# Optimization experiments

Hardware: AMD Instinct MI355X
Metric: run time of the kernel (lower is better)

## Reference

```python
import jax, jax.numpy as jnp
import numpy as np

B, T, H = 8, 512, 1024
DC = 8            # concept_dim_total = 6 + 2
DIN = H + DC      # 1032
V, L = 8, 4       # op_vocab_size, prog_len


def setup_inputs() -> dict:
    key = jax.random.key(0)
    ks = jax.random.split(key, 20)
    s = 0.02
    inp = {
        "x": jax.random.normal(ks[0], (B, T, H), dtype=jnp.float32),
        # concept classifier heads
        "W_tt": jax.random.normal(ks[1], (6, H), dtype=jnp.float32) * s,
        "b_tt": jnp.zeros((6,), jnp.float32),
        "W_pol": jax.random.normal(ks[2], (2, H), dtype=jnp.float32) * s,
        "b_pol": jnp.zeros((2,), jnp.float32),
        # program generator
        "W_c2h": jax.random.normal(ks[3], (H, DIN), dtype=jnp.float32) * s,
        "b_c2h": jnp.zeros((H,), jnp.float32),
        "W_ih": jax.random.normal(ks[4], (3 * H, DIN), dtype=jnp.float32) * s,
        "W_hh": jax.random.normal(ks[5], (3 * H, H), dtype=jnp.float32) * s,
        "b_ih": jnp.zeros((3 * H,), jnp.float32),
        "b_hh": jnp.zeros((3 * H,), jnp.float32),
        "W_proj": jax.random.normal(ks[6], (V, H), dtype=jnp.float32) * s,
        "b_proj": jnp.zeros((V,), jnp.float32),
        # op library: num_ops stacked Linear(DIN->H)-GELU-Linear(H->H)
        "W1": jax.random.normal(ks[7], (V, H, DIN), dtype=jnp.float32) * s,
        "b1": jnp.zeros((V, H), jnp.float32),
        "W2": jax.random.normal(ks[8], (V, H, H), dtype=jnp.float32) * s,
        "b2": jnp.zeros((V, H), jnp.float32),
    }
    return inp


def _forward(x, W_tt, b_tt, W_pol, b_pol, W_c2h, b_c2h, W_ih, W_hh, b_ih, b_hh,
             W_proj, b_proj, W1, b1, W2, b2):
    # concept classifier
    tt = x @ W_tt.T + b_tt              # (B,T,6)
    pol = x @ W_pol.T + b_pol           # (B,T,2)
    concept_feats = jnp.concatenate([tt, pol], axis=-1)  # (B,T,8)
    concept_summary = jnp.concatenate([tt.mean(axis=1), pol.mean(axis=1)], axis=-1)  # (B,8)
    pooled = x.mean(axis=1)             # (B,H)
    context = jnp.concatenate([pooled, concept_summary], axis=-1)  # (B,DIN)

    # program generator: GRU with zero inputs, h0 from context (PyTorch gate eqs)
    h0 = context @ W_c2h.T + b_c2h      # (B,H)
    zero_in = jnp.zeros((context.shape[0], DIN), x.dtype)
    gi = zero_in @ W_ih.T + b_ih        # (B,3H); zero-input contribution = bias
    gi_r, gi_z, gi_n = jnp.split(gi, 3, axis=-1)

    def gru_step(h, _):
        gh = h @ W_hh.T + b_hh
        gh_r, gh_z, gh_n = jnp.split(gh, 3, axis=-1)
        r = jax.nn.sigmoid(gi_r + gh_r)
        z = jax.nn.sigmoid(gi_z + gh_z)
        n = jnp.tanh(gi_n + r * gh_n)
        h_new = (1.0 - z) * n + z * h
        return h_new, h_new

    _, hs = jax.lax.scan(gru_step, h0, None, length=L)   # (L,B,H)
    rnn_out = jnp.transpose(hs, (1, 0, 2))               # (B,L,H)
    program_logits = rnn_out @ W_proj.T + b_proj         # (B,L,V)

    # op library: outputs are identical across L, so compute each op once and
    # average the softmax weights over L (exact same math as expand+mean).
    x_aug = jnp.concatenate([x, concept_feats], axis=-1)           # (B,T,DIN)
    hmid = jax.nn.gelu(jnp.einsum('btd,vhd->btvh', x_aug, W1) + b1, approximate=False)
    op_out = jnp.einsum('btvh,voh->btvo', hmid, W2) + b2           # (B,T,V,H)
    w = jax.nn.softmax(program_logits, axis=-1).mean(axis=1)       # (B,V)
    out = jnp.einsum('btvd,bv->btd', op_out, w)                    # (B,T,H)
    return out, program_logits, tt, pol, pooled


def reference(x, W_tt, b_tt, W_pol, b_pol, W_c2h, b_c2h, W_ih, W_hh, b_ih, b_hh,
              W_proj, b_proj, W1, b1, W2, b2):
    return _forward(x, W_tt, b_tt, W_pol, b_pol, W_c2h, b_c2h, W_ih, W_hh,
                    b_ih, b_hh, W_proj, b_proj, W1, b1, W2, b2)
```

## Files before the change

kernel.cpp:

```cpp
#include <hip/hip_runtime.h>
#include <hip/hip_bf16.h>
#include <math.h>

typedef __bf16 bf16;
typedef __bf16 bf16x8 __attribute__((ext_vector_type(8)));
typedef float f32x4 __attribute__((ext_vector_type(4)));


__device__ __forceinline__ float wsum(float v) {
#pragma unroll
  for (int off = 32; off; off >>= 1) v += __shfl_xor(v, off, 64);
  return v;
}

__device__ __forceinline__ void g2l16(const bf16* g, bf16* l) {
  __builtin_amdgcn_global_load_lds(
      (__attribute__((address_space(1))) void*)g,
      (__attribute__((address_space(3))) void*)l, 16, 0, 0);
}

__device__ __forceinline__ bf16x8 pack8(float4 a, float4 b) {
  bf16x8 r;
  r[0] = (bf16)a.x; r[1] = (bf16)a.y; r[2] = (bf16)a.z; r[3] = (bf16)a.w;
  r[4] = (bf16)b.x; r[5] = (bf16)b.y; r[6] = (bf16)b.z; r[7] = (bf16)b.w;
  return r;
}

__device__ __forceinline__ float gelu_fast(float x) {
  float s = __builtin_fabsf(x) * 0.70710678118654752f;
  float t = __builtin_amdgcn_rcpf(__builtin_fmaf(0.3275911f, s, 1.0f));
  float p = __builtin_fmaf(t, 1.061405429f, -1.453152027f);
  p = __builtin_fmaf(t, p, 1.421413741f);
  p = __builtin_fmaf(t, p, -0.284496736f);
  p = __builtin_fmaf(t, p, 0.254829592f);
  float e = exp2f(s * s * -1.4426950408889634f);
  float erf_abs = __builtin_fmaf(-p * t, e, 1.0f);
  return __builtin_fmaf(0.5f * __builtin_fabsf(x), erf_abs, 0.5f * x);
}

__global__ void k_cvt(const float* __restrict__ s, bf16* __restrict__ d, long n) {
  long stride = (long)gridDim.x * blockDim.x;
  for (long i = (long)blockIdx.x * blockDim.x + threadIdx.x; i * 8 < n; i += stride) {
    long e = i * 8;
    if (e + 8 <= n) {
      float4 a = *(const float4*)(s + e);
      float4 b = *(const float4*)(s + e + 4);
      *(bf16x8*)(d + e) = pack8(a, b);
    } else {
      for (long j = e; j < n; j++) d[j] = (bf16)s[j];
    }
  }
}

__global__ void k_xext(const float* __restrict__ x, const float* __restrict__ feats,
                       bf16* __restrict__ xbE, int H, int KE, int DC, long BT) {
  int wave = threadIdx.x >> 6, lane = threadIdx.x & 63;
  long m = (long)blockIdx.x * 4 + wave;
  if (m >= BT) return;
  const float* xp = x + m * H;
  bf16* dp = xbE + m * KE;
  for (int e = lane * 8; e + 8 <= H; e += 512) {
    float4 a = *(const float4*)(xp + e);
    float4 b = *(const float4*)(xp + e + 4);
    *(bf16x8*)(dp + e) = pack8(a, b);
  }
  int pad = KE - H;
  if (lane < pad)
    dp[H + lane] = (lane < DC) ? (bf16)feats[m * DC + lane] : (bf16)0.f;
}

__global__ void k_w1ext(const float* __restrict__ W1, bf16* __restrict__ W1bE,
                        int H, int DIN, int KE, int DC, long N2) {
  int wave = threadIdx.x >> 6, lane = threadIdx.x & 63;
  long n = (long)blockIdx.x * 4 + wave;
  if (n >= N2) return;
  const float* sp = W1 + n * DIN;
  bf16* dp = W1bE + n * KE;
  for (int e = lane * 8; e + 8 <= H; e += 512) {
    float4 a = *(const float4*)(sp + e);
    float4 b = *(const float4*)(sp + e + 4);
    *(bf16x8*)(dp + e) = pack8(a, b);
  }
  int pad = KE - H;
  if (lane < pad)
    dp[H + lane] = (lane < DC) ? (bf16)sp[H + lane] : (bf16)0.f;
}

template <int DCT>
__global__ void k_feats_t(const float* __restrict__ x,
                          const float* __restrict__ Wtt, const float* __restrict__ btt,
                          const float* __restrict__ Wpol, const float* __restrict__ bpol,
                          float* __restrict__ out_tt, float* __restrict__ out_pol,
                          float* __restrict__ feats,
                          int H, int T, int BT, int C1, int C2) {
  int wave = threadIdx.x >> 6, lane = threadIdx.x & 63;
  int site = blockIdx.x * 4 + wave;
  if (site >= BT) return;
  const float* xp = x + (size_t)site * H;
  const float* wp[DCT];
#pragma unroll
  for (int c = 0; c < DCT; c++)
    wp[c] = (c < C1) ? (Wtt + (size_t)c * H) : (Wpol + (size_t)(c - C1) * H);
  float acc[DCT];
#pragma unroll
  for (int c = 0; c < DCT; c++) acc[c] = 0.f;
  for (int k = lane * 4; k < H; k += 256) {
    float4 xv = *(const float4*)(xp + k);
#pragma unroll
    for (int c = 0; c < DCT; c++) {
      float4 wv4 = *(const float4*)(wp[c] + k);
      acc[c] += xv.x * wv4.x + xv.y * wv4.y + xv.z * wv4.z + xv.w * wv4.w;
    }
  }
#pragma unroll
  for (int c = 0; c < DCT; c++) acc[c] = wsum(acc[c]);
  if (lane == 0) {
#pragma unroll
    for (int c = 0; c < DCT; c++) {
      float val = acc[c] + (c < C1 ? btt[c] : bpol[c - C1]);
      if (c < C1) out_tt[(size_t)site * C1 + c] = val;
      else        out_pol[(size_t)site * C2 + (c - C1)] = val;
      feats[(size_t)site * DCT + c] = val;
    }
  }
}

__global__ void k_feats_g(const float* __restrict__ x,
                          const float* __restrict__ Wtt, const float* __restrict__ btt,
                          const float* __restrict__ Wpol, const float* __restrict__ bpol,
                          float* __restrict__ out_tt, float* __restrict__ out_pol,
                          float* __restrict__ feats,
                          int H, int T, int BT, int C1, int C2) {
  int wave = threadIdx.x >> 6, lane = threadIdx.x & 63;
  int site = blockIdx.x * 4 + wave;
  if (site >= BT) return;
  int DC = C1 + C2;
  const float* xp = x + (size_t)site * H;
  for (int c = 0; c < DC; c++) {
    const float* wr = (c < C1) ? (Wtt + (size_t)c * H) : (Wpol + (size_t)(c - C1) * H);
    float a = 0.f;
    for (int k = lane; k < H; k += 64) a += xp[k] * wr[k];
    a = wsum(a);
    if (lane == 0) {
      float val = a + (c < C1 ? btt[c] : bpol[c - C1]);
      if (c < C1) out_tt[(size_t)site * C1 + c] = val;
      else        out_pol[(size_t)site * C2 + (c - C1)] = val;
      feats[(size_t)site * DC + c] = val;
    }
  }
}

__global__ void k_fsum(const float* __restrict__ feats, float* __restrict__ fsum,
                       int T, int DC, int BDC) {
  int wave = threadIdx.x >> 6, lane = threadIdx.x & 63;
  int r = blockIdx.x * 4 + wave;
  if (r >= BDC) return;
  int b = r / DC, c = r % DC;
  const float* p = feats + ((size_t)b * T) * DC + c;
  float a = 0.f;
  for (int t = lane; t < T; t += 64) a += p[(size_t)t * DC];
  a = wsum(a);
  if (lane == 0) fsum[r] = a / (float)T;
}

__global__ void k_pool(const float* __restrict__ x, float* __restrict__ pooled,
                       int H, int T, int tsplit) {
  int hBlocks = (H + 255) / 256;
  int bs = blockIdx.x / tsplit, ts = blockIdx.x % tsplit;
  int b = bs / hBlocks;
  int h = (bs % hBlocks) * 256 + threadIdx.x;
  if (h >= H) return;
  int tlo = (int)(((long)T * ts) / tsplit), thi = (int)(((long)T * (ts + 1)) / tsplit);
  const float* p = x + (size_t)b * T * H + h;
  float s = 0.f;
  for (int t = tlo; t < thi; t++) s += p[(size_t)t * H];
  atomicAdd(&pooled[(size_t)b * H + h], s / (float)T);
}

__global__ void k_ctx_h0(const float* __restrict__ Wc2h, const float* __restrict__ bc2h,
                         const float* __restrict__ pooled, const float* __restrict__ fmean,
                         float* __restrict__ h0, float* __restrict__ out_pool,
                         int H, int DIN, int B, int DC) {
  int wave = threadIdx.x >> 6, lane = threadIdx.x & 63;
  int r = blockIdx.x * 4 + wave;
  if (r >= B * H) return;
  int b = r / H, j = r % H;
  const float* wrow = Wc2h + (size_t)j * DIN;
  float a = 0.f;
  for (int k = lane; k < DIN; k += 64) {
    float cv = (k < H) ? pooled[(size_t)b * H + k] : fmean[b * DC + (k - H)];
    a += cv * wrow[k];
  }
  a = wsum(a);
  if (lane == 0) {
    h0[r] = a + bc2h[j];
    out_pool[r] = pooled[r];
  }
}

__global__ void k_gru(const float* __restrict__ hin, const float* __restrict__ Whh,
                      const float* __restrict__ bih, const float* __restrict__ bhh,
                      float* __restrict__ hout, float* __restrict__ hsl,
                      int H, int B) {
  int wave = threadIdx.x >> 6, lane = threadIdx.x & 63;
  int r = blockIdx.x * 4 + wave;
  if (r >= B * H) return;
  int b = r / H, j = r % H;
  const float* h = hin + (size_t)b * H;
  const float* w0 = Whh + (size_t)j * H;
  const float* w1 = Whh + (size_t)(H + j) * H;
  const float* w2 = Whh + (size_t)(2 * H + j) * H;
  float ar = 0, az = 0, an = 0;
  for (int k = lane; k < H; k += 64) {
    float hv = h[k];
    ar += hv * w0[k];
    az += hv * w1[k];
    an += hv * w2[k];
  }
  ar = wsum(ar); az = wsum(az); an = wsum(an);
  if (lane == 0) {
    float ghr = ar + bhh[j];
    float ghz = az + bhh[H + j];
    float ghn = an + bhh[2 * H + j];
    float rg = 1.f / (1.f + expf(-(bih[j] + ghr)));
    float zg = 1.f / (1.f + expf(-(bih[H + j] + ghz)));
    float ng = tanhf(bih[2 * H + j] + rg * ghn);
    float hn = (1.f - zg) * ng + zg * h[j];
    hout[r] = hn;
    hsl[r] = hn;
  }
}

__global__ void k_logits(const float* __restrict__ hs, const float* __restrict__ Wproj,
                         const float* __restrict__ bproj, float* __restrict__ logits,
                         float* __restrict__ out_log, int H, int B, int L, int V) {
  int wave = threadIdx.x >> 6, lane = threadIdx.x & 63;
  int r = blockIdx.x * 4 + wave;
  if (r >= B * L * V) return;
  int b = r / (L * V), rem = r % (L * V), l = rem / V, u = rem % V;
  const float* h = hs + ((size_t)l * B + b) * H;
  const float* w = Wproj + (size_t)u * H;
  float a = 0.f;
  for (int k = lane; k < H; k += 64) a += h[k] * w[k];
  a = wsum(a);
  if (lane == 0) {
    a += bproj[u];
    int idx = (b * L + l) * V + u;
    logits[idx] = a;
    out_log[idx] = a;
  }
}

__global__ void k_wmix(const float* __restrict__ logits, const float* __restrict__ b2,
                       float* __restrict__ wv, float* __restrict__ wb2,
                       int B, int L, int V, int H) {
  __shared__ float sm[2048];
  __shared__ float wsh[512];
  int t = threadIdx.x;
  if (t < B * L) {
    const float* lg = logits + t * V;
    float mx = lg[0];
    for (int u = 1; u < V; u++) mx = fmaxf(mx, lg[u]);
    float s = 0.f;
    for (int u = 0; u < V; u++) s += expf(lg[u] - mx);
    for (int u = 0; u < V; u++) sm[t * V + u] = expf(lg[u] - mx) / s;
  }
  __syncthreads();
  if (t < B * V) {
    int b = t / V, u = t % V;
    float a = 0.f;
    for (int l = 0; l < L; l++) a += sm[(b * L + l) * V + u];
    a /= (float)L;
    wsh[t] = a;
    wv[t] = a;
  }
  __syncthreads();
  for (int idx = t; idx < B * H; idx += 256) {
    int b = idx / H, o = idx % H;
    float a = 0.f;
    for (int u = 0; u < V; u++) a += wsh[b * V + u] * b2[(size_t)u * H + o];
    wb2[idx] = a;
  }
}

__global__ __launch_bounds__(256, 2) void gemm1_mfma(
    const bf16* __restrict__ A, const bf16* __restrict__ Bb, bf16* __restrict__ hmid,
    const float* __restrict__ b1, const float* __restrict__ wv,
    int rows, long moff, int KE, int H, int N, int T, int V) {
  __shared__ __align__(16) bf16 As[128 * 64];
  __shared__ __align__(16) bf16 Bs[128 * 64];
  const int wave = threadIdx.x >> 6, lane = threadIdx.x & 63;
  int bx = blockIdx.x, by = blockIdx.y;
  if (gridDim.x == 64 && (gridDim.y & 3) == 0) {
    int f = by * 64 + bx;
    int xcd = f & 7, q = f >> 3;
    int cs = q >> 5, t = q & 31;
    bx = xcd * 8 + (t & 7);
    by = cs * 4 + (t >> 3);
  }
  const int m0 = by * 128, n0 = bx * 128;
  const int mw = (wave >> 1) * 64, nw = (wave & 1) * 64;
  const int rr = lane >> 3;
  const int srcOff = ((lane & 7) ^ rr) << 3;
  const int rA = lane & 15, q4 = lane >> 4;
  f32x4 acc[4][4];
#pragma unroll
  for (int i = 0; i < 4; i++)
#pragma unroll
    for (int j = 0; j < 4; j++) acc[i][j] = (f32x4){0.f, 0.f, 0.f, 0.f};

  int arow[4], brow[4];
#pragma unroll
  for (int t = 0; t < 4; ++t) {
    int r = wave * 32 + t * 8 + rr;
    arow[t] = (m0 + r < rows) ? (m0 + r) : (rows - 1);
    brow[t] = (n0 + r < N) ? (n0 + r) : (N - 1);
  }

  for (int k0 = 0; k0 < KE; k0 += 64) {
    __syncthreads();
#pragma unroll
    for (int t = 0; t < 4; ++t) {
      int c = wave * 4 + t;
      g2l16(A + (size_t)arow[t] * KE + k0 + srcOff, &As[c * 512]);
      g2l16(Bb + (size_t)brow[t] * KE + k0 + srcOff, &Bs[c * 512]);
    }
    __syncthreads();
#pragma unroll
    for (int kk = 0; kk < 2; ++kk) {
      bf16x8 af[4], bfr[4];
#pragma unroll
      for (int i = 0; i < 4; i++) {
        int row = mw + i * 16 + rA;
        af[i] = *(const bf16x8*)&As[row * 64 + ((((kk << 2) + q4) ^ (row & 7)) << 3)];
      }
#pragma unroll
      for (int j = 0; j < 4; j++) {
        int row = nw + j * 16 + rA;
        bfr[j] = *(const bf16x8*)&Bs[row * 64 + ((((kk << 2) + q4) ^ (row & 7)) << 3)];
      }
#pragma unroll
      for (int i = 0; i < 4; i++)
#pragma unroll
        for (int j = 0; j < 4; j++)
          acc[i][j] = __builtin_amdgcn_mfma_f32_16x16x32_bf16(af[i], bfr[j], acc[i][j], 0, 0, 0);
    }
  }

  int vj[4];
  float b1j[4];
#pragma unroll
  for (int j = 0; j < 4; j++) {
    int n = n0 + nw + j * 16 + rA;
    if (n >= N) n = N - 1;
    vj[j] = n / H;
    b1j[j] = b1[n];
  }
  int bBase = ((T & 127) == 0) ? (int)((moff + m0) / T) : -1;
  float wfac[4];
#pragma unroll
  for (int j = 0; j < 4; j++)
    wfac[j] = (bBase >= 0) ? wv[bBase * V + vj[j]] : 0.f;
#pragma unroll
  for (int i = 0; i < 4; i++) {
#pragma unroll
    for (int r = 0; r < 4; r++) {
      int m = m0 + mw + i * 16 + q4 * 4 + r;
      if (m >= rows) continue;
      long gm = moff + m;
      int bb = (bBase >= 0) ? bBase : (int)(gm / T);
#pragma unroll
      for (int j = 0; j < 4; j++) {
        int n = n0 + nw + j * 16 + rA;
        if (n >= N) continue;
        float val = gelu_fast(acc[i][j][r] + b1j[j]);
        float wf = (bBase >= 0) ? wfac[j] : wv[bb * V + vj[j]];
        hmid[(size_t)m * N + n] = (bf16)(val * wf);
      }
    }
  }
}

__global__ __launch_bounds__(256, 2) void gemm2_mfma(
    const bf16* __restrict__ A, const bf16* __restrict__ W2b, float* __restrict__ part,
    long partStride, int rows, int H, int K, int kchunk) {
  __shared__ __align__(16) bf16 As[128 * 64];
  __shared__ __align__(16) bf16 Bs[128 * 64];
  const int wave = threadIdx.x >> 6, lane = threadIdx.x & 63;
  int bx = blockIdx.x, by = blockIdx.y;
  if (gridDim.x == 8 && (gridDim.y & 31) == 0) {
    int f = by * 8 + bx;
    int xcd = f & 7, q = f >> 3;
    int cs = q >> 5, t = q & 31;
    bx = t & 7;
    by = (xcd + (cs << 3)) * 4 + (t >> 3);
  }
  const int m0 = by * 128, n0 = bx * 128;
  const int mw = (wave >> 1) * 64, nw = (wave & 1) * 64;
  const int rr = lane >> 3;
  const int srcOff = ((lane & 7) ^ rr) << 3;
  const int rA = lane & 15, q4 = lane >> 4;
  int kz0 = blockIdx.z * kchunk;
  int kz1 = kz0 + kchunk; if (kz1 > K) kz1 = K;
  if (kz0 >= K) return;
  f32x4 acc[4][4];
#pragma unroll
  for (int i = 0; i < 4; i++)
#pragma unroll
    for (int j = 0; j < 4; j++) acc[i][j] = (f32x4){0.f, 0.f, 0.f, 0.f};

  int arow[4], brow[4];
#pragma unroll
  for (int t = 0; t < 4; ++t) {
    int r = wave * 32 + t * 8 + rr;
    arow[t] = (m0 + r < rows) ? (m0 + r) : (rows - 1);
    brow[t] = (n0 + r < H) ? (n0 + r) : (H - 1);
  }

  int kv = kz0 / H, kh = kz0 % H;
  for (int k0 = kz0; k0 < kz1; k0 += 64) {
    const bf16* Bk = W2b + (size_t)kv * H * H + kh;
    __syncthreads();
#pragma unroll
    for (int t = 0; t < 4; ++t) {
      int c = wave * 4 + t;
      g2l16(A + (size_t)arow[t] * K + k0 + srcOff, &As[c * 512]);
      g2l16(Bk + (size_t)brow[t] * H + srcOff, &Bs[c * 512]);
    }
    __syncthreads();
#pragma unroll
    for (int kk = 0; kk < 2; ++kk) {
      bf16x8 af[4], bfr[4];
#pragma unroll
      for (int i = 0; i < 4; i++) {
        int row = mw + i * 16 + rA;
        af[i] = *(const bf16x8*)&As[row * 64 + ((((kk << 2) + q4) ^ (row & 7)) << 3)];
      }
#pragma unroll
      for (int j = 0; j < 4; j++) {
        int row = nw + j * 16 + rA;
        bfr[j] = *(const bf16x8*)&Bs[row * 64 + ((((kk << 2) + q4) ^ (row & 7)) << 3)];
      }
#pragma unroll
      for (int i = 0; i < 4; i++)
#pragma unroll
        for (int j = 0; j < 4; j++)
          acc[i][j] = __builtin_amdgcn_mfma_f32_16x16x32_bf16(af[i], bfr[j], acc[i][j], 0, 0, 0);
    }
    kh += 64;
    if (kh >= H) { kh = 0; kv++; }
  }

  float* pz = part + (size_t)blockIdx.z * partStride;
#pragma unroll
  for (int i = 0; i < 4; i++) {
#pragma unroll
    for (int r = 0; r < 4; r++) {
      int m = m0 + mw + i * 16 + q4 * 4 + r;
      if (m >= rows) continue;
#pragma unroll
      for (int j = 0; j < 4; j++) {
        int n = n0 + nw + j * 16 + rA;
        if (n >= H) continue;
        pz[(size_t)m * H + n] = acc[i][j][r];
      }
    }
  }
}

__global__ void k_red(const float* __restrict__ part, const float* __restrict__ wb2,
                      float* __restrict__ outY, long moff, int rows, long partStride,
                      int H, int T, int ZS) {
  int wave = threadIdx.x >> 6, lane = threadIdx.x & 63;
  long m = (long)blockIdx.x * 4 + wave;
  if (m >= rows) return;
  long gm = moff + m;
  int b = (int)(gm / T);
  const float* w = wb2 + (size_t)b * H;
  float* d = outY + (size_t)gm * H;
  for (int e = lane * 4; e + 4 <= H; e += 256) {
    float4 s = *(const float4*)(w + e);
    for (int z = 0; z < ZS; z++) {
      float4 p = *(const float4*)(part + (size_t)z * partStride + (size_t)m * H + e);
      s.x += p.x; s.y += p.y; s.z += p.z; s.w += p.w;
    }
    *(float4*)(d + e) = s;
  }
}

extern "C" void kernel_launch(void* const* d_in, const int* in_sizes, int n_in,
                              void* d_out, int out_size, void* d_ws, size_t ws_size,
                              hipStream_t stream) {
  const float* x      = (const float*)d_in[0];
  const float* W_tt   = (const float*)d_in[1];
  const float* b_tt   = (const float*)d_in[2];
  const float* W_pol  = (const float*)d_in[3];
  const float* b_pol  = (const float*)d_in[4];
  const float* W_c2h  = (const float*)d_in[5];
  const float* b_c2h  = (const float*)d_in[6];
  const float* W_hh   = (const float*)d_in[8];
  const float* b_ih   = (const float*)d_in[9];
  const float* b_hh   = (const float*)d_in[10];
  const float* W_proj = (const float*)d_in[11];
  const float* b_proj = (const float*)d_in[12];
  const float* W1     = (const float*)d_in[13];
  const float* b1     = (const float*)d_in[14];
  const float* W2     = (const float*)d_in[15];
  const float* b2     = (const float*)d_in[16];
  float* out = (float*)d_out;
  char* ws = (char*)d_ws;

  const int C1 = in_sizes[2];
  const int C2 = in_sizes[4];
  const int H  = in_sizes[1] / C1;
  const int DC = C1 + C2;
  const int DIN = H + DC;
  const int V  = in_sizes[12];
  const long BT = (long)in_sizes[0] / H;
  long R = (long)out_size - BT * (long)(H + DC);
  int B = 0, L = 0;
  for (int Lc = 1; Lc <= 32; ++Lc) {
    long den = (long)Lc * V + H;
    if (R % den == 0) {
      long Bc = R / den;
      if (Bc >= 1 && BT % Bc == 0) {
        if (B == 0 || Lc == 4) { B = (int)Bc; L = Lc; }
        if (Lc == 4) break;
      }
    }
  }
  if (B == 0) { B = 8; L = 4; }
  const int T = (int)(BT / B);
  const long N2 = (long)V * H;
  const int KE = H + 64;
  const int ZS = 4;

  size_t o = 0;
  auto alloc = [&](size_t bytes) { size_t r = o; o = (o + bytes + 255) & ~(size_t)255; return r; };
  float* feats  = (float*)(ws + alloc((size_t)BT * DC * 4));
  size_t off_pooled = alloc((size_t)B * H * 4);
  float* pooled = (float*)(ws + off_pooled);
  float* fsum   = (float*)(ws + alloc((size_t)B * DC * 4));
  float* hbuf   = (float*)(ws + alloc((size_t)2 * B * H * 4));
  float* hs     = (float*)(ws + alloc((size_t)L * B * H * 4));
  float* logits = (float*)(ws + alloc((size_t)B * L * V * 4));
  float* wv     = (float*)(ws + alloc((size_t)B * V * 4));
  float* wb2    = (float*)(ws + alloc((size_t)B * H * 4));
  bf16* xbE  = (bf16*)(ws + alloc((size_t)BT * KE * 2));
  bf16* W1bE = (bf16*)(ws + alloc((size_t)N2 * KE * 2));
  bf16* W2b  = (bf16*)(ws + alloc((size_t)N2 * H * 2));
  size_t off_hmid = alloc(0);
  long rowBytes = N2 * 2 + (long)ZS * H * 4;
  long avail = (long)ws_size - (long)off_hmid;
  long Mc = ((avail / rowBytes) / 128) * 128;
  long bt128 = ((BT + 127) / 128) * 128;
  if (Mc > bt128) Mc = bt128;
  if (Mc < 128) Mc = 128;
  bf16* hmid = (bf16*)(ws + off_hmid);
  float* part = (float*)(ws + off_hmid + (size_t)Mc * N2 * 2);
  long partStride = Mc * (long)H;

  float* out_y    = out;
  float* out_log  = out_y + (size_t)BT * H;
  float* out_tt   = out_log + (size_t)B * L * V;
  float* out_pol  = out_tt + (size_t)BT * C1;
  float* out_pool = out_pol + (size_t)BT * C2;

  hipMemsetAsync(ws + off_pooled, 0, (size_t)B * H * 4, stream);

  k_cvt<<<4096, 256, 0, stream>>>(W2, W2b, N2 * (long)H);
  if (DC == 8 && (H & 1023) == 0)
    k_feats_t<8><<<(int)((BT + 3) / 4), 256, 0, stream>>>(x, W_tt, b_tt, W_pol, b_pol,
                                                          out_tt, out_pol, feats,
                                                          H, T, (int)BT, C1, C2);
  else
    k_feats_g<<<(int)((BT + 3) / 4), 256, 0, stream>>>(x, W_tt, b_tt, W_pol, b_pol,
                                                       out_tt, out_pol, feats,
                                                       H, T, (int)BT, C1, C2);
  k_fsum<<<(B * DC + 3) / 4, 256, 0, stream>>>(feats, fsum, T, DC, B * DC);
  k_xext<<<(int)((BT + 3) / 4), 256, 0, stream>>>(x, feats, xbE, H, KE, DC, BT);
  k_w1ext<<<(int)((N2 + 3) / 4), 256, 0, stream>>>(W1, W1bE, H, DIN, KE, DC, N2);
  int hBlocks = (H + 255) / 256;
  k_pool<<<B * hBlocks * 8, 256, 0, stream>>>(x, pooled, H, T, 8);
  k_ctx_h0<<<(B * H + 3) / 4, 256, 0, stream>>>(W_c2h, b_c2h, pooled, fsum,
                                                hbuf, out_pool, H, DIN, B, DC);
  float* hA = hbuf;
  float* hB = hbuf + (size_t)B * H;
  for (int l = 0; l < L; ++l) {
    k_gru<<<(B * H + 3) / 4, 256, 0, stream>>>((l & 1) ? hB : hA, W_hh, b_ih, b_hh,
                                               (l & 1) ? hA : hB, hs + (size_t)l * B * H,
                                               H, B);
  }
  k_logits<<<(B * L * V + 3) / 4, 256, 0, stream>>>(hs, W_proj, b_proj, logits,
                                                    out_log, H, B, L, V);
  k_wmix<<<1, 256, 0, stream>>>(logits, b2, wv, wb2, B, L, V, H);

  int kchunk = (int)((((N2 / ZS) + 63) / 64) * 64);
  for (long moff = 0; moff < BT; moff += Mc) {
    int rows = (int)(((BT - moff) < Mc) ? (BT - moff) : Mc);
    dim3 g1((unsigned)((N2 + 127) / 128), (unsigned)((rows + 127) / 128));
    dim3 g2((unsigned)((H + 127) / 128), (unsigned)((rows + 127) / 128), ZS);
    gemm1_mfma<<<g1, 256, 0, stream>>>(xbE + (size_t)moff * KE, W1bE, hmid, b1, wv,
                                       rows, moff, KE, H, (int)N2, T, V);
    gemm2_mfma<<<g2, 256, 0, stream>>>(hmid, W2b, part, partStride,
                                       rows, H, (int)N2, kchunk);
    k_red<<<(int)((rows + 3) / 4), 256, 0, stream>>>(part, wb2, out_y, moff, rows,
                                                     partStride, H, T, ZS);
  }
}
```

Measured before the change: 462.9 us.

## Fuse front-end kernels: concept heads with x bf16 conversion, weight casts, pooling stats

Merges the concept-classifier dot products with the bf16 conversion of x into one pass, so x is read once for both. It also packs the W1 and W2 bf16 conversions into a single launch and the mean-pool and feature-mean reductions into another. The aim is to cut launch count and a redundant full read of x. The cost is larger, branchier kernels with more register pressure in the fused feature kernel.

```diff
diff --git a/kernel.cpp b/kernel.cpp
--- a/kernel.cpp
+++ b/kernel.cpp
@@ -38,91 +38,50 @@
   return __builtin_fmaf(0.5f * __builtin_fabsf(x), erf_abs, 0.5f * x);
 }
 
-__global__ void k_cvt(const float* __restrict__ s, bf16* __restrict__ d, long n) {
-  long stride = (long)gridDim.x * blockDim.x;
-  for (long i = (long)blockIdx.x * blockDim.x + threadIdx.x; i * 8 < n; i += stride) {
-    long e = i * 8;
-    if (e + 8 <= n) {
-      float4 a = *(const float4*)(s + e);
-      float4 b = *(const float4*)(s + e + 4);
-      *(bf16x8*)(d + e) = pack8(a, b);
-    } else {
-      for (long j = e; j < n; j++) d[j] = (bf16)s[j];
-    }
-  }
-}
-
-__global__ void k_xext(const float* __restrict__ x, const float* __restrict__ feats,
-                       bf16* __restrict__ xbE, int H, int KE, int DC, long BT) {
+template <int DCT>
+__global__ void k_front_t(const float* __restrict__ x,
+                          const float* __restrict__ Wtt, const float* __restrict__ btt,
+                          const float* __restrict__ Wpol, const float* __restrict__ bpol,
+                          float* __restrict__ out_tt, float* __restrict__ out_pol,
+                          float* __restrict__ feats, bf16* __restrict__ xbE,
+                          int H, int KE, long BT, int C1, int C2) {
   int wave = threadIdx.x >> 6, lane = threadIdx.x & 63;
   long m = (long)blockIdx.x * 4 + wave;
   if (m >= BT) return;
   const float* xp = x + m * H;
   bf16* dp = xbE + m * KE;
+  const float* wp[DCT];
+#pragma unroll
+  for (int c = 0; c < DCT; c++)
+    wp[c] = (c < C1) ? (Wtt + (size_t)c * H) : (Wpol + (size_t)(c - C1) * H);
+  float acc[DCT];
+#pragma unroll
+  for (int c = 0; c < DCT; c++) acc[c] = 0.f;
   for (int e = lane * 8; e + 8 <= H; e += 512) {
     float4 a = *(const float4*)(xp + e);
     float4 b = *(const float4*)(xp + e + 4);
     *(bf16x8*)(dp + e) = pack8(a, b);
+#pragma unroll
+    for (int c = 0; c < DCT; c++) {
+      float4 wa = *(const float4*)(wp[c] + e);
+      float4 wb = *(const float4*)(wp[c] + e + 4);
+      acc[c] += a.x * wa.x + a.y * wa.y + a.z * wa.z + a.w * wa.w +
+                b.x * wb.x + b.y * wb.y + b.z * wb.z + b.w * wb.w;
+    }
+  }
+#pragma unroll
+  for (int c = 0; c < DCT; c++) acc[c] = wsum(acc[c]);
+  float fv = 0.f;
+#pragma unroll
+  for (int c = 0; c < DCT; c++) fv = (lane == c) ? acc[c] : fv;
+  if (lane < DCT) {
+    fv += (lane < C1) ? btt[lane] : bpol[lane - C1];
+    if (lane < C1) out_tt[m * C1 + lane] = fv;
+    else           out_pol[m * C2 + (lane - C1)] = fv;
+    feats[m * DCT + lane] = fv;
   }
   int pad = KE - H;
-  if (lane < pad)
-    dp[H + lane] = (lane < DC) ? (bf16)feats[m * DC + lane] : (bf16)0.f;
-}
-
-__global__ void k_w1ext(const float* __restrict__ W1, bf16* __restrict__ W1bE,
-                        int H, int DIN, int KE, int DC, long N2) {
-  int wave = threadIdx.x >> 6, lane = threadIdx.x & 63;
-  long n = (long)blockIdx.x * 4 + wave;
-  if (n >= N2) return;
-  const float* sp = W1 + n * DIN;
-  bf16* dp = W1bE + n * KE;
-  for (int e = lane * 8; e + 8 <= H; e += 512) {
-    float4 a = *(const float4*)(sp + e);
-    float4 b = *(const float4*)(sp + e + 4);
-    *(bf16x8*)(dp + e) = pack8(a, b);
-  }
-  int pad = KE - H;
-  if (lane < pad)
-    dp[H + lane] = (lane < DC) ? (bf16)sp[H + lane] : (bf16)0.f;
-}
-
-template <int DCT>
-__global__ void k_feats_t(const float* __restrict__ x,
-                          const float* __restrict__ Wtt, const float* __restrict__ btt,
-                          const float* __restrict__ Wpol, const float* __restrict__ bpol,
-                          float* __restrict__ out_tt, float* __restrict__ out_pol,
-                          float* __restrict__ feats,
-                          int H, int T, int BT, int C1, int C2) {
-  int wave = threadIdx.x >> 6, lane = threadIdx.x & 63;
-  int site = blockIdx.x * 4 + wave;
-  if (site >= BT) return;
-  const float* xp = x + (size_t)site * H;
-  const float* wp[DCT];
-#pragma unroll
-  for (int c = 0; c < DCT; c++)
-    wp[c] = (c < C1) ? (Wtt + (size_t)c * H) : (Wpol + (size_t)(c - C1) * H);
-  float acc[DCT];
-#pragma unroll
-  for (int c = 0; c < DCT; c++) acc[c] = 0.f;
-  for (int k = lane * 4; k < H; k += 256) {
-    float4 xv = *(const float4*)(xp + k);
-#pragma unroll
-    for (int c = 0; c < DCT; c++) {
-      float4 wv4 = *(const float4*)(wp[c] + k);
-      acc[c] += xv.x * wv4.x + xv.y * wv4.y + xv.z * wv4.z + xv.w * wv4.w;
-    }
-  }
-#pragma unroll
-  for (int c = 0; c < DCT; c++) acc[c] = wsum(acc[c]);
-  if (lane == 0) {
-#pragma unroll
-    for (int c = 0; c < DCT; c++) {
-      float val = acc[c] + (c < C1 ? btt[c] : bpol[c - C1]);
-      if (c < C1) out_tt[(size_t)site * C1 + c] = val;
-      else        out_pol[(size_t)site * C2 + (c - C1)] = val;
-      feats[(size_t)site * DCT + c] = val;
-    }
-  }
+  if (lane < pad) dp[H + lane] = (lane < DCT) ? (bf16)fv : (bf16)0.f;
 }
 
 __global__ void k_feats_g(const float* __restrict__ x,
@@ -150,31 +109,81 @@
   }
 }
 
-__global__ void k_fsum(const float* __restrict__ feats, float* __restrict__ fsum,
-                       int T, int DC, int BDC) {
-  int wave = threadIdx.x >> 6, lane = threadIdx.x & 63;
-  int r = blockIdx.x * 4 + wave;
-  if (r >= BDC) return;
-  int b = r / DC, c = r % DC;
-  const float* p = feats + ((size_t)b * T) * DC + c;
-  float a = 0.f;
-  for (int t = lane; t < T; t += 64) a += p[(size_t)t * DC];
-  a = wsum(a);
-  if (lane == 0) fsum[r] = a / (float)T;
-}
-
-__global__ void k_pool(const float* __restrict__ x, float* __restrict__ pooled,
-                       int H, int T, int tsplit) {
-  int hBlocks = (H + 255) / 256;
-  int bs = blockIdx.x / tsplit, ts = blockIdx.x % tsplit;
-  int b = bs / hBlocks;
-  int h = (bs % hBlocks) * 256 + threadIdx.x;
-  if (h >= H) return;
-  int tlo = (int)(((long)T * ts) / tsplit), thi = (int)(((long)T * (ts + 1)) / tsplit);
-  const float* p = x + (size_t)b * T * H + h;
-  float s = 0.f;
-  for (int t = tlo; t < thi; t++) s += p[(size_t)t * H];
-  atomicAdd(&pooled[(size_t)b * H + h], s / (float)T);
+__global__ void k_xext(const float* __restrict__ x, const float* __restrict__ feats,
+                       bf16* __restrict__ xbE, int H, int KE, int DC, long BT) {
+  int wave = threadIdx.x >> 6, lane = threadIdx.x & 63;
+  long m = (long)blockIdx.x * 4 + wave;
+  if (m >= BT) return;
+  const float* xp = x + m * H;
+  bf16* dp = xbE + m * KE;
+  for (int e = lane * 8; e + 8 <= H; e += 512) {
+    float4 a = *(const float4*)(xp + e);
+    float4 b = *(const float4*)(xp + e + 4);
+    *(bf16x8*)(dp + e) = pack8(a, b);
+  }
+  int pad = KE - H;
+  if (lane < pad)
+    dp[H + lane] = (lane < DC) ? (bf16)feats[m * DC + lane] : (bf16)0.f;
+}
+
+__global__ void k_prep(const float* __restrict__ W1, bf16* __restrict__ W1bE,
+                       const float* __restrict__ W2, bf16* __restrict__ W2b,
+                       int H, int DIN, int KE, int DC, long N2, int nW1, long nCvtThreads) {
+  int wave = threadIdx.x >> 6, lane = threadIdx.x & 63;
+  if (blockIdx.x < (unsigned)nW1) {
+    long n = (long)blockIdx.x * 4 + wave;
+    if (n >= N2) return;
+    const float* sp = W1 + n * DIN;
+    bf16* dp = W1bE + n * KE;
+    for (int e = lane * 8; e + 8 <= H; e += 512) {
+      float4 a = *(const float4*)(sp + e);
+      float4 b = *(const float4*)(sp + e + 4);
+      *(bf16x8*)(dp + e) = pack8(a, b);
+    }
+    int pad = KE - H;
+    if (lane < pad)
+      dp[H + lane] = (lane < DC) ? (bf16)sp[H + lane] : (bf16)0.f;
+  } else {
+    long n = N2 * (long)H;
+    for (long i = (long)(blockIdx.x - nW1) * 256 + threadIdx.x; i * 8 < n;
+         i += nCvtThreads) {
+      long e = i * 8;
+      if (e + 8 <= n) {
+        float4 a = *(const float4*)(W2 + e);
+        float4 b = *(const float4*)(W2 + e + 4);
+        *(bf16x8*)(W2b + e) = pack8(a, b);
+      } else {
+        for (long j = e; j < n; j++) W2b[j] = (bf16)W2[j];
+      }
+    }
+  }
+}
+
+__global__ void k_stats(const float* __restrict__ x, float* __restrict__ pooled,
+                        const float* __restrict__ feats, float* __restrict__ fsum,
+                        int H, int T, int tsplit, int DC, int BDC, int poolBlocks) {
+  int wave = threadIdx.x >> 6, lane = threadIdx.x & 63;
+  if (blockIdx.x < (unsigned)poolBlocks) {
+    int hBlocks = (H + 255) / 256;
+    int bs = blockIdx.x / tsplit, ts = blockIdx.x % tsplit;
+    int b = bs / hBlocks;
+    int h = (bs % hBlocks) * 256 + threadIdx.x;
+    if (h >= H) return;
+    int tlo = (int)(((long)T * ts) / tsplit), thi = (int)(((long)T * (ts + 1)) / tsplit);
+    const float* p = x + (size_t)b * T * H + h;
+    float s = 0.f;
+    for (int t = tlo; t < thi; t++) s += p[(size_t)t * H];
+    atomicAdd(&pooled[(size_t)b * H + h], s / (float)T);
+  } else {
+    int r = (blockIdx.x - poolBlocks) * 4 + wave;
+    if (r >= BDC) return;
+    int b = r / DC, c = r % DC;
+    const float* p = feats + ((size_t)b * T) * DC + c;
+    float a = 0.f;
+    for (int t = lane; t < T; t += 64) a += p[(size_t)t * DC];
+    a = wsum(a);
+    if (lane == 0) fsum[r] = a / (float)T;
+  }
 }
 
 __global__ void k_ctx_h0(const float* __restrict__ Wc2h, const float* __restrict__ bc2h,
@@ -568,20 +577,25 @@
 
   hipMemsetAsync(ws + off_pooled, 0, (size_t)B * H * 4, stream);
 
-  k_cvt<<<4096, 256, 0, stream>>>(W2, W2b, N2 * (long)H);
-  if (DC == 8 && (H & 1023) == 0)
-    k_feats_t<8><<<(int)((BT + 3) / 4), 256, 0, stream>>>(x, W_tt, b_tt, W_pol, b_pol,
-                                                          out_tt, out_pol, feats,
-                                                          H, T, (int)BT, C1, C2);
-  else
+  int nW1 = (int)((N2 + 3) / 4);
+  int nCvt = 1024;
+  k_prep<<<nW1 + nCvt, 256, 0, stream>>>(W1, W1bE, W2, W2b, H, DIN, KE, DC, N2,
+                                         nW1, (long)nCvt * 256);
+  if (DC == 8 && (H & 1023) == 0) {
+    k_front_t<8><<<(int)((BT + 3) / 4), 256, 0, stream>>>(x, W_tt, b_tt, W_pol, b_pol,
+                                                          out_tt, out_pol, feats, xbE,
+                                                          H, KE, BT, C1, C2);
+  } else {
     k_feats_g<<<(int)((BT + 3) / 4), 256, 0, stream>>>(x, W_tt, b_tt, W_pol, b_pol,
                                                        out_tt, out_pol, feats,
                                                        H, T, (int)BT, C1, C2);
-  k_fsum<<<(B * DC + 3) / 4, 256, 0, stream>>>(feats, fsum, T, DC, B * DC);
-  k_xext<<<(int)((BT + 3) / 4), 256, 0, stream>>>(x, feats, xbE, H, KE, DC, BT);
-  k_w1ext<<<(int)((N2 + 3) / 4), 256, 0, stream>>>(W1, W1bE, H, DIN, KE, DC, N2);
+    k_xext<<<(int)((BT + 3) / 4), 256, 0, stream>>>(x, feats, xbE, H, KE, DC, BT);
+  }
   int hBlocks = (H + 255) / 256;
-  k_pool<<<B * hBlocks * 8, 256, 0, stream>>>(x, pooled, H, T, 8);
+  int poolBlocks = B * hBlocks * 8;
+  int fsumBlocks = (B * DC + 3) / 4;
+  k_stats<<<poolBlocks + fsumBlocks, 256, 0, stream>>>(x, pooled, feats, fsum,
+                                                       H, T, 8, DC, B * DC, poolBlocks);
   k_ctx_h0<<<(B * H + 3) / 4, 256, 0, stream>>>(W_c2h, b_c2h, pooled, fsum,
                                                 hbuf, out_pool, H, DIN, B, DC);
   float* hA = hbuf;
```

After: 454.9 us. No clear change (-1.7%).
